# Kernel tuning notes

Hardware: AMD Instinct MI355X
Metric: run time of the kernel (lower is better)

## Reference

```python
import jax, jax.numpy as jnp
import numpy as np


def setup_inputs() -> dict:
    key = jax.random.key(0)
    k1, k2, k3, k4 = jax.random.split(key, 4)
    B, H_in, W_in = 512, 128, 64
    H_out, W_out, K = 256, 64, 4
    x = jax.random.normal(k1, (B, H_in, W_in), dtype=jnp.float32)
    mask = jax.random.randint(k2, (H_out, K), 0, H_in, dtype=jnp.int64)
    # stacked per-group weights (width_out, width_in*K) and biases (width_out,)
    W = jax.random.normal(k3, (H_out, W_out, W_in * K), dtype=jnp.float32) * 0.05
    b = jax.random.normal(k4, (H_out, W_out), dtype=jnp.float32) * 0.05
    return {"x": x, "mask": mask, "W": W, "b": b}


def reference(x, mask, W, b):
    # x: [B, H_in, W_in]; mask: [H_out, K]; W: [H_out, W_out, K*W_in]; b: [H_out, W_out]
    B = x.shape[0]
    H_out, K = mask.shape
    # gather rows per group: [B, H_out, K, W_in]
    gathered = x[:, mask, :]
    # flatten kernel window: [B, H_out, K*W_in]
    gathered = gathered.reshape(B, H_out, -1)
    # per-group linear: out[b,h,o] = sum_d gathered[b,h,d] * W[h,o,d] + b[h,o]
    out = jnp.einsum('bhd,hod->bho', gathered, W) + b[None, :, :]
    return out  # [B, H_out, W_out]
```

## Files before the change

kernel.cpp:

```cpp
#include <hip/hip_runtime.h>

constexpr int H_OUT = 256;
constexpr int D     = 256;

typedef __bf16 bf16x8 __attribute__((ext_vector_type(8)));
typedef float  f32x16 __attribute__((ext_vector_type(16)));

__device__ __forceinline__ ushort f2bf(float f) {
    uint u = __float_as_uint(f);
    u = (u + 0x7FFFu + ((u >> 16) & 1u)) >> 16;
    return (ushort)u;
}
__device__ __forceinline__ uint pack2(float a, float b) {
    return (uint)f2bf(a) | ((uint)f2bf(b) << 16);
}
__device__ __forceinline__ uint2 pack4(float4 v) {
    uint2 r; r.x = pack2(v.x, v.y); r.y = pack2(v.z, v.w); return r;
}
__device__ __forceinline__ bf16x8 packfrag(float4 lo, float4 hi4) {
    uint4 o;
    o.x = pack2(lo.x, lo.y);  o.y = pack2(lo.z, lo.w);
    o.z = pack2(hi4.x, hi4.y); o.w = pack2(hi4.z, hi4.w);
    return __builtin_bit_cast(bf16x8, o);
}

__global__ __launch_bounds__(256, 4) void sparse_linear_v6(
    const float* __restrict__ x,
    const int*   __restrict__ mask,
    const float* __restrict__ W,
    const float* __restrict__ bias,
    float*       __restrict__ out)
{
    const int bx   = blockIdx.x;
    const int h    = ((bx >> 5) << 3) | (bx & 7);
    const int bq   = (bx >> 3) & 3;
    const int tid  = threadIdx.x;
    const int lane = tid & 63, wid = tid >> 6;
    const int rowl = lane & 31, hi = lane >> 5;

    __shared__ float4 Wls[64 * 32];

    int mq[4];
    #pragma unroll
    for (int q = 0; q < 4; ++q) mq[q] = mask[h * 4 + q];

    const float* xb = x + (size_t)(bq * 128 + wid * 32 + rowl) * (128 * 64);

    float4 pa0, pb0, pa1, pb1;
    {
        const int k00 = hi * 8;
        const float* p0 = xb + mq[0] * 64 + k00;
        pa0 = ((const float4*)p0)[0]; pb0 = ((const float4*)p0)[1];
        const int k01 = 16 + hi * 8;
        const float* p1 = xb + mq[0] * 64 + k01;
        pa1 = ((const float4*)p1)[0]; pb1 = ((const float4*)p1)[1];
    }

    {
        const int c    = tid & 63;
        const int wrow = tid >> 6;
        const float4* wsrc = (const float4*)(W + (size_t)h * 64 * D);
        #pragma unroll
        for (int p = 0; p < 16; ++p) {
            const int R = p * 4 + wrow;
            const float4 v = wsrc[(size_t)R * 64 + c];
            *((uint2*)&Wls[R * 32 + ((c >> 1) ^ (R & 15))] + (c & 1)) = pack4(v);
        }
    }
    __syncthreads();

    const int xv = rowl & 15;
    f32x16 acc0 = {}, acc1 = {};

    #pragma unroll
    for (int ks = 0; ks < 16; ++ks) {
        const bf16x8 a = (ks & 1) ? packfrag(pa1, pb1) : packfrag(pa0, pb0);

        if (ks + 2 < 16) {
            const int kn = (ks + 2) * 16 + hi * 8;
            const float* pn = xb + mq[kn >> 6] * 64 + (kn & 63);
            if (ks & 1) { pa1 = ((const float4*)pn)[0]; pb1 = ((const float4*)pn)[1]; }
            else        { pa0 = ((const float4*)pn)[0]; pb0 = ((const float4*)pn)[1]; }
        }

        const int s = ks * 2 + hi;
        const bf16x8 b0 = __builtin_bit_cast(bf16x8, Wls[rowl * 32 + (s ^ xv)]);
        const bf16x8 b1 = __builtin_bit_cast(bf16x8, Wls[(32 + rowl) * 32 + (s ^ xv)]);
        acc0 = __builtin_amdgcn_mfma_f32_32x32x16_bf16(a, b0, acc0, 0, 0, 0);
        acc1 = __builtin_amdgcn_mfma_f32_32x32x16_bf16(a, b1, acc1, 0, 0, 0);
    }

    const float bv0 = bias[h * 64 + rowl];
    const float bv1 = bias[h * 64 + 32 + rowl];
    #pragma unroll
    for (int reg = 0; reg < 16; ++reg) {
        const int rl = (reg & 3) + 8 * (reg >> 2) + 4 * hi;
        const size_t b = (size_t)bq * 128 + wid * 32 + rl;
        float* o = out + (b * H_OUT + h) * 64;
        o[rowl]      = acc0[reg] + bv0;
        o[32 + rowl] = acc1[reg] + bv1;
    }
}

extern "C" void kernel_launch(void* const* d_in, const int* in_sizes, int n_in,
                              void* d_out, int out_size, void* d_ws, size_t ws_size,
                              hipStream_t stream) {
    const float* x    = (const float*)d_in[0];
    const int*   mask = (const int*)d_in[1];
    const float* W    = (const float*)d_in[2];
    const float* bias = (const float*)d_in[3];
    float* out = (float*)d_out;

    dim3 grid(1024);
    dim3 block(256);
    sparse_linear_v6<<<grid, block, 0, stream>>>(x, mask, W, bias, out);
}
```

Before: 104.1 us.

## Pre-convert x and W to bf16 in a separate pass with MFMA-friendly layout

Adds a prep kernel that converts x and W to bf16 once and writes x into a transposed, fragment-ordered layout in the workspace. The main kernel then loads ready-made bf16 fragments with one coalesced 16-byte load per lane, with no per-use packing, and copies W tiles into shared memory without conversion. This removes the redundant conversion work (each x row is gathered by about 8 groups) and halves the bytes read in the gather. The cost is a second launch plus a full read of x and W and a write of their bf16 copies to the workspace.

After: 102.5 us. No clear change (-1.5%).

```diff
diff --git a/kernel.cpp b/kernel.cpp
--- a/kernel.cpp
+++ b/kernel.cpp
@@ -14,22 +14,47 @@
 __device__ __forceinline__ uint pack2(float a, float b) {
     return (uint)f2bf(a) | ((uint)f2bf(b) << 16);
 }
-__device__ __forceinline__ uint2 pack4(float4 v) {
-    uint2 r; r.x = pack2(v.x, v.y); r.y = pack2(v.z, v.w); return r;
-}
-__device__ __forceinline__ bf16x8 packfrag(float4 lo, float4 hi4) {
-    uint4 o;
-    o.x = pack2(lo.x, lo.y);  o.y = pack2(lo.z, lo.w);
-    o.z = pack2(hi4.x, hi4.y); o.w = pack2(hi4.z, hi4.w);
-    return __builtin_bit_cast(bf16x8, o);
+
+__global__ __launch_bounds__(256) void prep_bf16(
+    const float* __restrict__ x,
+    const float* __restrict__ W,
+    ushort* __restrict__ xbt,
+    ushort* __restrict__ Wb)
+{
+    const int bx = blockIdx.x;
+    const int t  = (bx & 1023) * 256 + threadIdx.x;
+    if (bx < 1024) {
+        const int rowl = t & 31, w16 = (t >> 5) & 3, hin = (t >> 7) & 127, b5 = t >> 14;
+        const float4* src = (const float4*)(x + (((size_t)(b5 * 32 + rowl) * 128 + hin) * 64 + w16 * 16));
+        const float4 v0 = src[0], v1 = src[1], v2 = src[2], v3 = src[3];
+        uint4 lo, hi4;
+        lo.x  = pack2(v0.x, v0.y); lo.y  = pack2(v0.z, v0.w);
+        lo.z  = pack2(v1.x, v1.y); lo.w  = pack2(v1.z, v1.w);
+        hi4.x = pack2(v2.x, v2.y); hi4.y = pack2(v2.z, v2.w);
+        hi4.z = pack2(v3.x, v3.y); hi4.w = pack2(v3.z, v3.w);
+        const size_t d16 = ((size_t)(b5 * 128 + hin) * 8 + w16 * 2) * 32 + rowl;
+        ((uint4*)xbt)[d16]      = lo;
+        ((uint4*)xbt)[d16 + 32] = hi4;
+    } else {
+        const size_t u = (size_t)t * 16;
+        const float4* src = (const float4*)(W + u);
+        const float4 v0 = src[0], v1 = src[1], v2 = src[2], v3 = src[3];
+        uint4 o0, o1;
+        o0.x = pack2(v0.x, v0.y); o0.y = pack2(v0.z, v0.w);
+        o0.z = pack2(v1.x, v1.y); o0.w = pack2(v1.z, v1.w);
+        o1.x = pack2(v2.x, v2.y); o1.y = pack2(v2.z, v2.w);
+        o1.z = pack2(v3.x, v3.y); o1.w = pack2(v3.z, v3.w);
+        ((uint4*)Wb)[2 * t]     = o0;
+        ((uint4*)Wb)[2 * t + 1] = o1;
+    }
 }
 
-__global__ __launch_bounds__(256, 4) void sparse_linear_v6(
-    const float* __restrict__ x,
-    const int*   __restrict__ mask,
-    const float* __restrict__ W,
-    const float* __restrict__ bias,
-    float*       __restrict__ out)
+__global__ __launch_bounds__(256, 4) void sparse_linear_v7(
+    const ushort* __restrict__ xbt,
+    const ushort* __restrict__ Wb,
+    const int*    __restrict__ mask,
+    const float*  __restrict__ bias,
+    float*        __restrict__ out)
 {
     const int bx   = blockIdx.x;
     const int h    = ((bx >> 5) << 3) | (bx & 7);
@@ -37,6 +62,7 @@
     const int tid  = threadIdx.x;
     const int lane = tid & 63, wid = tid >> 6;
     const int rowl = lane & 31, hi = lane >> 5;
+    const int b5   = bq * 4 + wid;
 
     __shared__ float4 Wls[64 * 32];
 
@@ -44,27 +70,20 @@
     #pragma unroll
     for (int q = 0; q < 4; ++q) mq[q] = mask[h * 4 + q];
 
-    const float* xb = x + (size_t)(bq * 128 + wid * 32 + rowl) * (128 * 64);
+    const uint4* xb16 = (const uint4*)xbt;
+    #define XIDX(ks) (((size_t)(b5 * 128 + mq[(ks) >> 2]) * 8 + ((ks) & 3) * 2 + hi) * 32 + rowl)
 
-    float4 pa0, pb0, pa1, pb1;
-    {
-        const int k00 = hi * 8;
-        const float* p0 = xb + mq[0] * 64 + k00;
-        pa0 = ((const float4*)p0)[0]; pb0 = ((const float4*)p0)[1];
-        const int k01 = 16 + hi * 8;
-        const float* p1 = xb + mq[0] * 64 + k01;
-        pa1 = ((const float4*)p1)[0]; pb1 = ((const float4*)p1)[1];
-    }
+    uint4 pa0 = xb16[XIDX(0)];
+    uint4 pa1 = xb16[XIDX(1)];
 
     {
-        const int c    = tid & 63;
-        const int wrow = tid >> 6;
-        const float4* wsrc = (const float4*)(W + (size_t)h * 64 * D);
+        const int c2 = tid & 31, R0 = tid >> 5;
+        const uint4* wsrc = (const uint4*)(Wb + (size_t)h * 64 * D);
         #pragma unroll
-        for (int p = 0; p < 16; ++p) {
-            const int R = p * 4 + wrow;
-            const float4 v = wsrc[(size_t)R * 64 + c];
-            *((uint2*)&Wls[R * 32 + ((c >> 1) ^ (R & 15))] + (c & 1)) = pack4(v);
+        for (int p = 0; p < 8; ++p) {
+            const int R = p * 8 + R0;
+            const uint4 v = wsrc[R * 32 + c2];
+            Wls[R * 32 + (c2 ^ (R & 15))] = __builtin_bit_cast(float4, v);
         }
     }
     __syncthreads();
@@ -74,13 +93,11 @@
 
     #pragma unroll
     for (int ks = 0; ks < 16; ++ks) {
-        const bf16x8 a = (ks & 1) ? packfrag(pa1, pb1) : packfrag(pa0, pb0);
+        const bf16x8 a = __builtin_bit_cast(bf16x8, (ks & 1) ? pa1 : pa0);
 
         if (ks + 2 < 16) {
-            const int kn = (ks + 2) * 16 + hi * 8;
-            const float* pn = xb + mq[kn >> 6] * 64 + (kn & 63);
-            if (ks & 1) { pa1 = ((const float4*)pn)[0]; pb1 = ((const float4*)pn)[1]; }
-            else        { pa0 = ((const float4*)pn)[0]; pb0 = ((const float4*)pn)[1]; }
+            const uint4 pn = xb16[XIDX(ks + 2)];
+            if (ks & 1) pa1 = pn; else pa0 = pn;
         }
 
         const int s = ks * 2 + hi;
@@ -89,6 +106,7 @@
         acc0 = __builtin_amdgcn_mfma_f32_32x32x16_bf16(a, b0, acc0, 0, 0, 0);
         acc1 = __builtin_amdgcn_mfma_f32_32x32x16_bf16(a, b1, acc1, 0, 0, 0);
     }
+    #undef XIDX
 
     const float bv0 = bias[h * 64 + rowl];
     const float bv1 = bias[h * 64 + 32 + rowl];
@@ -109,9 +127,10 @@
     const int*   mask = (const int*)d_in[1];
     const float* W    = (const float*)d_in[2];
     const float* bias = (const float*)d_in[3];
-    float* out = (float*)d_out;
+    float*  out = (float*)d_out;
+    ushort* xbt = (ushort*)d_ws;
+    ushort* Wb  = (ushort*)((char*)d_ws + 8388608);
 
-    dim3 grid(1024);
-    dim3 block(256);
-    sparse_linear_v6<<<grid, block, 0, stream>>>(x, mask, W, bias, out);
+    prep_bf16<<<dim3(2048), dim3(256), 0, stream>>>(x, W, xbt, Wb);
+    sparse_linear_v7<<<dim3(1024), dim3(256), 0, stream>>>(xbt, Wb, mask, bias, out);
 }
```
